# Kernel optimization log

Measured on AMD Instinct MI355X. Metric: run time of the kernel, lower is better.

Reference implementation:

```python
import jax, jax.numpy as jnp
import numpy as np
from jax import lax

K = 3
K2 = K * K
PAD = 1          # dcn padding = kernel_size // 2
OFF_DIL = 2      # offset conv dilation & padding
GN_GROUPS = 32
EPS = 1e-5


def setup_inputs() -> dict:
    key = jax.random.key(0)
    ks = jax.random.split(key, 4)
    B, C1, C2, H, W = 4, 256, 256, 64, 64
    x = jax.random.normal(ks[0], (B, C1, H, W), jnp.float32)
    # offset conv params (zero-init in module; small random here so deformable
    # sampling is genuinely irregular)
    w_off = jax.random.normal(ks[1], (3 * K2, C1, K, K), jnp.float32) * 0.01
    b_off = jax.random.normal(ks[2], (3 * K2,), jnp.float32) * 0.01
    # dcn weight, bias=False
    w_dcn = jax.random.normal(ks[3], (C2, C1, K, K), jnp.float32) * (1.0 / np.sqrt(C1 * K2))
    gamma = jnp.ones((C2,), jnp.float32)
    beta = jnp.zeros((C2,), jnp.float32)
    return {"x": x, "w_off": w_off, "b_off": b_off, "w_dcn": w_dcn,
            "gamma": gamma, "beta": beta}


def _dcnv2_block(x, w_off, b_off, w_dcn, gamma, beta):
    B, C, H, W = x.shape
    C2 = w_dcn.shape[0]

    # ---- offset/mask prediction: 3x3 conv, dilation=2, padding=2, stride=1 ----
    out_off = lax.conv_general_dilated(
        x, w_off, window_strides=(1, 1), padding=[(OFF_DIL, OFF_DIL)] * 2,
        rhs_dilation=(OFF_DIL, OFF_DIL),
        dimension_numbers=("NCHW", "OIHW", "NCHW"))
    out_off = out_off + b_off[None, :, None, None]

    offset = jnp.nan_to_num(jnp.clip(out_off[:, :2 * K2], -64.0, 64.0))
    mask = jax.nn.sigmoid(out_off[:, 2 * K2:])                     # [B,K2,H,W]

    off = offset.reshape(B, K2, 2, H, W)                            # (dy,dx) pairs per kernel pt
    dy, dx = off[:, :, 0], off[:, :, 1]                             # [B,K2,H,W]

    # ---- sampling positions: p0 + pk + offset (stride=1, pad=1, dil=1) ----
    ii = (jnp.arange(K2) // K).astype(jnp.float32)                  # kernel row
    jj = (jnp.arange(K2) % K).astype(jnp.float32)                   # kernel col
    yo = jnp.arange(H, dtype=jnp.float32)
    xo = jnp.arange(W, dtype=jnp.float32)
    py = yo[None, None, :, None] - PAD + ii[None, :, None, None] + dy   # [B,K2,H,W]
    px = xo[None, None, None, :] - PAD + jj[None, :, None, None] + dx

    y0 = jnp.floor(py)
    x0 = jnp.floor(px)
    wy = py - y0                                                    # frac weights
    wx = px - x0
    y0i = y0.astype(jnp.int32)
    x0i = x0.astype(jnp.int32)

    xf = x.reshape(B, C, H * W)

    def gather(yi, xi):
        # zero outside image (torchvision zero-padding bilinear semantics)
        valid = (yi >= 0) & (yi < H) & (xi >= 0) & (xi < W)
        idx = jnp.clip(yi, 0, H - 1) * W + jnp.clip(xi, 0, W - 1)   # [B,K2,H,W]
        v = jax.vmap(lambda xb, ib: xb[:, ib])(xf, idx.reshape(B, -1))  # [B,C,K2*H*W]
        v = v.reshape(B, C, K2, H, W)
        return v * valid[:, None].astype(x.dtype)

    v00 = gather(y0i, x0i)
    v01 = gather(y0i, x0i + 1)
    v10 = gather(y0i + 1, x0i)
    v11 = gather(y0i + 1, x0i + 1)

    wy_ = wy[:, None]
    wx_ = wx[:, None]
    samp = (v00 * (1 - wy_) * (1 - wx_) + v01 * (1 - wy_) * wx_
            + v10 * wy_ * (1 - wx_) + v11 * wy_ * wx_)              # [B,C,K2,H,W]
    samp = samp * mask[:, None]                                     # modulated (DCNv2)

    out = jnp.einsum("bckhw,dck->bdhw", samp, w_dcn.reshape(C2, C, K2))

    # ---- GroupNorm(32, C2) + SiLU ----
    G = GN_GROUPS
    o = out.reshape(B, G, C2 // G, H, W)
    mu = o.mean(axis=(2, 3, 4), keepdims=True)
    var = o.var(axis=(2, 3, 4), keepdims=True)
    o = (o - mu) * lax.rsqrt(var + EPS)
    out = o.reshape(B, C2, H, W) * gamma[None, :, None, None] + beta[None, :, None, None]
    return out * jax.nn.sigmoid(out)


def reference(x, w_off, b_off, w_dcn, gamma, beta):
    return _dcnv2_block(x, w_off, b_off, w_dcn, gamma, beta)
```

## Files before the change

kernel.cpp:

```cpp
#include <hip/hip_runtime.h>
#include <math.h>

#define HW 4096

typedef __attribute__((ext_vector_type(8))) short short8;
typedef __attribute__((ext_vector_type(4))) float f32x4;

static __device__ inline ushort f2bf(float f) {
    uint u = __builtin_bit_cast(uint, f);
    uint r = (u + 0x7fffu + ((u >> 16) & 1u)) >> 16;
    return (ushort)r;
}

__global__ __launch_bounds__(256) void k0_xt(const float* __restrict__ x, ushort* __restrict__ xt)
{
    const int blk = blockIdx.x;
    const int b = blk >> 6, h = blk & 63;
    __shared__ ushort tile[64 * 258];
    const float* xb = x + ((size_t)b * 256) * HW + h * 64;
    const int t = threadIdx.x;
    for (int e = t; e < 16384; e += 256) {
        const int c = e >> 6, j = e & 63;
        tile[j * 258 + c] = f2bf(xb[c * HW + j]);
    }
    __syncthreads();
    uint* xo = (uint*)(xt + ((size_t)b * HW + h * 64) * 256);
    for (int e = t; e < 8192; e += 256) {
        const int j = e >> 7, q = e & 127;
        xo[j * 128 + q] = *(const uint*)&tile[j * 258 + 2 * q];
    }
}

__global__ __launch_bounds__(256) void k0_wt(const float* __restrict__ w_dcn, ushort* __restrict__ wT)
{
    const int e = blockIdx.x * 256 + threadIdx.x;
    const int k = e >> 16, d = (e >> 8) & 255, c = e & 255;
    wT[e] = f2bf(w_dcn[(d * 256 + c) * 9 + k]);
}

__global__ __launch_bounds__(256) void k0_wo(const float* __restrict__ w_off, ushort* __restrict__ wA)
{
    const int e = blockIdx.x * 256 + threadIdx.x;
    const int k = e >> 13, r = e & 8191;
    const int oc = r >> 8, c = r & 255;
    const float v = (oc < 27) ? w_off[(oc * 256 + c) * 9 + k] : 0.f;
    wA[e] = f2bf(v);
}

__global__ __launch_bounds__(256) void k1_mfma(const ushort* __restrict__ xt,
    const ushort* __restrict__ wA, const float* __restrict__ b_off,
    float* __restrict__ offs, float* __restrict__ mk)
{
    const int bid = blockIdx.x;
    const int b = bid >> 6, h = bid & 63;
    const int t = threadIdx.x;
    const int lane = t & 63, wv = t >> 6;
    const int n = lane & 15, kq = lane >> 4;

    f32x4 acc0 = {0.f, 0.f, 0.f, 0.f}, acc1 = {0.f, 0.f, 0.f, 0.f};
    const ushort* xb = xt + ((size_t)b * HW) * 256;

    for (int k = 0; k < 9; ++k) {
        const int i = k / 3, j = k % 3;
        const int hh = h + 2 * (i - 1);
        if ((unsigned)hh >= 64u) continue;
        const int ww = wv * 16 + n + 2 * (j - 1);
        const bool vw = (unsigned)ww < 64u;
        const ushort* xrow  = xb + (hh * 64 + ww) * 256 + kq * 8;
        const ushort* wrow0 = wA + (k * 32 + n) * 256 + kq * 8;
        const ushort* wrow1 = wrow0 + 16 * 256;
#pragma unroll
        for (int c0 = 0; c0 < 256; c0 += 32) {
            short8 bfv = {0, 0, 0, 0, 0, 0, 0, 0};
            if (vw) bfv = *(const short8*)(xrow + c0);
            const short8 a0 = *(const short8*)(wrow0 + c0);
            const short8 a1 = *(const short8*)(wrow1 + c0);
            acc0 = __builtin_amdgcn_mfma_f32_16x16x32_bf16(a0, bfv, acc0, 0, 0, 0);
            acc1 = __builtin_amdgcn_mfma_f32_16x16x32_bf16(a1, bfv, acc1, 0, 0, 0);
        }
    }

    const int hw = h * 64 + wv * 16 + n;
#pragma unroll
    for (int r = 0; r < 4; ++r) {
        {
            const int oc = kq * 4 + r;
            float v = acc0[r] + b_off[oc];
            v = fminf(fmaxf(v, -64.f), 64.f);
            offs[(b * 18 + oc) * HW + hw] = v;
        }
        {
            const int oc = 16 + kq * 4 + r;
            const float v = acc1[r] + b_off[min(oc, 26)];
            if (oc < 18) {
                offs[(b * 18 + oc) * HW + hw] = fminf(fmaxf(v, -64.f), 64.f);
            } else if (oc < 27) {
                mk[(b * 9 + (oc - 18)) * HW + hw] = 1.f / (1.f + expf(-v));
            }
        }
    }
}

__global__ __launch_bounds__(1024) void k2_dcn(const ushort* __restrict__ xt, const ushort* __restrict__ wT,
    const float* __restrict__ offs, const float* __restrict__ mk, float* __restrict__ out)
{
    const int bid = blockIdx.x;
    const int wg = (bid & 7) * 32 + (bid >> 3);
    const int b = wg >> 6, h = wg & 63;
    const int t = threadIdx.x;

    __shared__ int4   cOff[576];
    __shared__ float4 cWgt[576];
    __shared__ ushort Alds[256 * 40];
    __shared__ ushort Slds[64 * 40];

    if (t < 576) {
        const int k = t >> 6, ww = t & 63;
        const float dy = offs[(b * 18 + 2 * k) * HW + h * 64 + ww];
        const float dx = offs[(b * 18 + 2 * k + 1) * HW + h * 64 + ww];
        const float mval = mk[(b * 9 + k) * HW + h * 64 + ww];
        const float py = (float)(h - 1 + k / 3) + dy;
        const float px = (float)(ww - 1 + k % 3) + dx;
        const float y0f = floorf(py), x0f = floorf(px);
        const float wy = py - y0f, wx = px - x0f;
        const int y0 = (int)y0f, x0 = (int)x0f;
        float w00 = (1.f - wy) * (1.f - wx) * mval, w01 = (1.f - wy) * wx * mval;
        float w10 = wy * (1.f - wx) * mval,         w11 = wy * wx * mval;
        const bool vy0 = (unsigned)y0 < 64u, vy1 = (unsigned)(y0 + 1) < 64u;
        const bool vx0 = (unsigned)x0 < 64u, vx1 = (unsigned)(x0 + 1) < 64u;
        if (!(vy0 && vx0)) w00 = 0.f;
        if (!(vy0 && vx1)) w01 = 0.f;
        if (!(vy1 && vx0)) w10 = 0.f;
        if (!(vy1 && vx1)) w11 = 0.f;
        const int y0c = min(max(y0, 0), 63), y1c = min(max(y0 + 1, 0), 63);
        const int x0c = min(max(x0, 0), 63), x1c = min(max(x0 + 1, 0), 63);
        cOff[t] = make_int4((y0c * 64 + x0c) * 512, (y0c * 64 + x1c) * 512,
                            (y1c * 64 + x0c) * 512, (y1c * 64 + x1c) * 512);
        cWgt[t] = make_float4(w00, w01, w10, w11);
    }

    f32x4 acc[4];
#pragma unroll
    for (int nf = 0; nf < 4; ++nf) acc[nf] = (f32x4){0.f, 0.f, 0.f, 0.f};

    const char* xc = (const char*)(xt + ((size_t)b * HW) * 256);
    const int lane = t & 63;
    const int d0 = (t >> 6) * 16;
    const int n0 = lane & 15, kb = (lane >> 4) * 8;
    const int sd = t >> 2, sq = t & 3;
    const int sw = t >> 4, sp = t & 15;

    __syncthreads();

    for (int k = 0; k < 9; ++k) {
        const int4   co = cOff[k * 64 + sw];
        const float4 cw = cWgt[k * 64 + sw];
        for (int c0 = 0; c0 < 256; c0 += 32) {
            __syncthreads();
            {
                const short8 av = *(const short8*)(wT + ((k * 256 + sd) * 256 + c0 + sq * 8));
                *(short8*)(&Alds[sd * 40 + sq * 8]) = av;
            }
            {
                const int cb = (c0 + sp * 2) * 2;
                const uint u00 = *(const uint*)(xc + (co.x + cb));
                const uint u01 = *(const uint*)(xc + (co.y + cb));
                const uint u10 = *(const uint*)(xc + (co.z + cb));
                const uint u11 = *(const uint*)(xc + (co.w + cb));
                const float sa = cw.x * __builtin_bit_cast(float, u00 << 16)
                               + cw.y * __builtin_bit_cast(float, u01 << 16)
                               + cw.z * __builtin_bit_cast(float, u10 << 16)
                               + cw.w * __builtin_bit_cast(float, u11 << 16);
                const float sb = cw.x * __builtin_bit_cast(float, u00 & 0xffff0000u)
                               + cw.y * __builtin_bit_cast(float, u01 & 0xffff0000u)
                               + cw.z * __builtin_bit_cast(float, u10 & 0xffff0000u)
                               + cw.w * __builtin_bit_cast(float, u11 & 0xffff0000u);
                ((uint*)Slds)[sw * 20 + sp] = (uint)f2bf(sa) | ((uint)f2bf(sb) << 16);
            }
            __syncthreads();
            const short8 af = *(const short8*)(&Alds[(d0 + n0) * 40 + kb]);
#pragma unroll
            for (int nf = 0; nf < 4; ++nf) {
                const short8 bf = *(const short8*)(&Slds[(nf * 16 + n0) * 40 + kb]);
                acc[nf] = __builtin_amdgcn_mfma_f32_16x16x32_bf16(af, bf, acc[nf], 0, 0, 0);
            }
        }
    }

    float* ob = out + ((size_t)b * 256) * HW + h * 64;
#pragma unroll
    for (int nf = 0; nf < 4; ++nf)
#pragma unroll
        for (int r = 0; r < 4; ++r) {
            const int d = d0 + (lane >> 4) * 4 + r;
            ob[d * HW + nf * 16 + n0] = acc[nf][r];
        }
}

__global__ __launch_bounds__(256) void k3_stats(const float* __restrict__ out, float* __restrict__ stats)
{
    const int bg = blockIdx.x;
    const float* p = out + (size_t)bg * 32768;
    float s = 0.f, s2 = 0.f;
    for (int i = threadIdx.x; i < 8192; i += 256) {
        float4 v = ((const float4*)p)[i];
        s  += v.x + v.y + v.z + v.w;
        s2 += v.x * v.x + v.y * v.y + v.z * v.z + v.w * v.w;
    }
    __shared__ float r1[256], r2[256];
    r1[threadIdx.x] = s; r2[threadIdx.x] = s2;
    __syncthreads();
    for (int st = 128; st > 0; st >>= 1) {
        if (threadIdx.x < st) {
            r1[threadIdx.x] += r1[threadIdx.x + st];
            r2[threadIdx.x] += r2[threadIdx.x + st];
        }
        __syncthreads();
    }
    if (threadIdx.x == 0) {
        const float mean = r1[0] / 32768.f;
        const float var  = r2[0] / 32768.f - mean * mean;
        stats[bg * 2]     = mean;
        stats[bg * 2 + 1] = rsqrtf(var + 1e-5f);
    }
}

__global__ __launch_bounds__(256) void k4_gn(float* __restrict__ out,
    const float* __restrict__ stats, const float* __restrict__ gamma, const float* __restrict__ beta)
{
    const int i4 = blockIdx.x * 256 + threadIdx.x;
    const int elem = i4 << 2;
    const int b = elem >> 20;
    const int ch = (elem >> 12) & 255;
    const int g = ch >> 3;
    const float mean = stats[(b * 32 + g) * 2];
    const float rstd = stats[(b * 32 + g) * 2 + 1];
    const float ga = gamma[ch], be = beta[ch];
    float4 v = ((float4*)out)[i4];
    float vv[4] = {v.x, v.y, v.z, v.w};
#pragma unroll
    for (int j = 0; j < 4; ++j) {
        const float o = (vv[j] - mean) * rstd * ga + be;
        vv[j] = o / (1.f + expf(-o));
    }
    ((float4*)out)[i4] = make_float4(vv[0], vv[1], vv[2], vv[3]);
}

extern "C" void kernel_launch(void* const* d_in, const int* in_sizes, int n_in,
                              void* d_out, int out_size, void* d_ws, size_t ws_size,
                              hipStream_t stream)
{
    const float* x     = (const float*)d_in[0];
    const float* w_off = (const float*)d_in[1];
    const float* b_off = (const float*)d_in[2];
    const float* w_dcn = (const float*)d_in[3];
    const float* gamma = (const float*)d_in[4];
    const float* beta  = (const float*)d_in[5];
    float* out = (float*)d_out;

    ushort* xt    = (ushort*)d_ws;
    float*  offs  = (float*)d_ws + 2097152;
    float*  mk    = offs + 294912;
    float*  stats = mk + 147456;
    ushort* wT    = (ushort*)(stats + 256);
    ushort* wA    = wT + 589824;

    hipLaunchKernelGGL(k0_xt,    dim3(256),  dim3(256),  0, stream, x, xt);
    hipLaunchKernelGGL(k0_wt,    dim3(2304), dim3(256),  0, stream, w_dcn, wT);
    hipLaunchKernelGGL(k0_wo,    dim3(288),  dim3(256),  0, stream, w_off, wA);
    hipLaunchKernelGGL(k1_mfma,  dim3(256),  dim3(256),  0, stream, xt, wA, b_off, offs, mk);
    hipLaunchKernelGGL(k2_dcn,   dim3(256),  dim3(1024), 0, stream, xt, wT, offs, mk, out);
    hipLaunchKernelGGL(k3_stats, dim3(128),  dim3(256),  0, stream, out, stats);
    hipLaunchKernelGGL(k4_gn,    dim3(4096), dim3(256),  0, stream, out, stats, gamma, beta);
}
```

Baseline: 209.9 us.

## Restructure DCN kernel with double-buffered sampled tiles, split-K offset conv, coalesced weight transpose

The main DCN kernel now samples a full 64x256 bf16 tile per kernel point into a double-buffered, XOR-swizzled LDS buffer. It builds the next point's tile while running MFMAs on the current one, so it needs one barrier per kernel point instead of two per 32-channel chunk. A-operand weights are read straight from global memory, and each wave computes a 32x64 output tile with 512 threads. The offset conv splits the channel reduction across two wave halves and reduces through LDS, and the weight transpose stages each output row in shared memory so reads are coalesced. In exchange, LDS use and register pressure per block go up, and the A-operand reads from global memory may not be reused well.

```diff
diff --git a/kernel.cpp b/kernel.cpp
--- a/kernel.cpp
+++ b/kernel.cpp
@@ -8,8 +8,10 @@
 
 static __device__ inline ushort f2bf(float f) {
     uint u = __builtin_bit_cast(uint, f);
-    uint r = (u + 0x7fffu + ((u >> 16) & 1u)) >> 16;
-    return (ushort)r;
+    return (ushort)((u + 0x7fffu + ((u >> 16) & 1u)) >> 16);
+}
+static __device__ inline float bf2f(ushort s) {
+    return __builtin_bit_cast(float, (uint)s << 16);
 }
 
 __global__ __launch_bounds__(256) void k0_xt(const float* __restrict__ x, ushort* __restrict__ xt)
@@ -33,9 +35,15 @@
 
 __global__ __launch_bounds__(256) void k0_wt(const float* __restrict__ w_dcn, ushort* __restrict__ wT)
 {
-    const int e = blockIdx.x * 256 + threadIdx.x;
-    const int k = e >> 16, d = (e >> 8) & 255, c = e & 255;
-    wT[e] = f2bf(w_dcn[(d * 256 + c) * 9 + k]);
+    const int d = blockIdx.x;
+    __shared__ float wl[2304];
+    const int t = threadIdx.x;
+    for (int i = t; i < 2304; i += 256) wl[i] = w_dcn[d * 2304 + i];
+    __syncthreads();
+    for (int i = t; i < 2304; i += 256) {
+        const int k = i >> 8, c = i & 255;
+        wT[k * 65536 + d * 256 + c] = f2bf(wl[c * 9 + k]);
+    }
 }
 
 __global__ __launch_bounds__(256) void k0_wo(const float* __restrict__ w_off, ushort* __restrict__ wA)
@@ -47,7 +55,7 @@
     wA[e] = f2bf(v);
 }
 
-__global__ __launch_bounds__(256) void k1_mfma(const ushort* __restrict__ xt,
+__global__ __launch_bounds__(512) void k1_mfma(const ushort* __restrict__ xt,
     const ushort* __restrict__ wA, const float* __restrict__ b_off,
     float* __restrict__ offs, float* __restrict__ mk)
 {
@@ -55,22 +63,25 @@
     const int b = bid >> 6, h = bid & 63;
     const int t = threadIdx.x;
     const int lane = t & 63, wv = t >> 6;
+    const int wq = wv & 3, chalf = wv >> 2;
     const int n = lane & 15, kq = lane >> 4;
+    __shared__ float red[4][64][8];
 
     f32x4 acc0 = {0.f, 0.f, 0.f, 0.f}, acc1 = {0.f, 0.f, 0.f, 0.f};
     const ushort* xb = xt + ((size_t)b * HW) * 256;
+    const int cb = chalf * 128;
 
     for (int k = 0; k < 9; ++k) {
         const int i = k / 3, j = k % 3;
         const int hh = h + 2 * (i - 1);
         if ((unsigned)hh >= 64u) continue;
-        const int ww = wv * 16 + n + 2 * (j - 1);
+        const int ww = wq * 16 + n + 2 * (j - 1);
         const bool vw = (unsigned)ww < 64u;
-        const ushort* xrow  = xb + (hh * 64 + ww) * 256 + kq * 8;
-        const ushort* wrow0 = wA + (k * 32 + n) * 256 + kq * 8;
+        const ushort* xrow  = xb + (hh * 64 + ww) * 256 + cb + kq * 8;
+        const ushort* wrow0 = wA + (k * 32 + n) * 256 + cb + kq * 8;
         const ushort* wrow1 = wrow0 + 16 * 256;
 #pragma unroll
-        for (int c0 = 0; c0 < 256; c0 += 32) {
+        for (int c0 = 0; c0 < 128; c0 += 32) {
             short8 bfv = {0, 0, 0, 0, 0, 0, 0, 0};
             if (vw) bfv = *(const short8*)(xrow + c0);
             const short8 a0 = *(const short8*)(wrow0 + c0);
@@ -80,47 +91,74 @@
         }
     }
 
-    const int hw = h * 64 + wv * 16 + n;
-#pragma unroll
-    for (int r = 0; r < 4; ++r) {
-        {
-            const int oc = kq * 4 + r;
-            float v = acc0[r] + b_off[oc];
-            v = fminf(fmaxf(v, -64.f), 64.f);
-            offs[(b * 18 + oc) * HW + hw] = v;
-        }
-        {
-            const int oc = 16 + kq * 4 + r;
-            const float v = acc1[r] + b_off[min(oc, 26)];
-            if (oc < 18) {
-                offs[(b * 18 + oc) * HW + hw] = fminf(fmaxf(v, -64.f), 64.f);
-            } else if (oc < 27) {
-                mk[(b * 9 + (oc - 18)) * HW + hw] = 1.f / (1.f + expf(-v));
-            }
-        }
-    }
-}
-
-__global__ __launch_bounds__(1024) void k2_dcn(const ushort* __restrict__ xt, const ushort* __restrict__ wT,
+    if (chalf == 1) {
+#pragma unroll
+        for (int r = 0; r < 4; ++r) {
+            red[wq][lane][r]     = acc0[r];
+            red[wq][lane][4 + r] = acc1[r];
+        }
+    }
+    __syncthreads();
+    if (chalf == 0) {
+#pragma unroll
+        for (int r = 0; r < 4; ++r) {
+            acc0[r] += red[wq][lane][r];
+            acc1[r] += red[wq][lane][4 + r];
+        }
+        const int hw = h * 64 + wq * 16 + n;
+#pragma unroll
+        for (int r = 0; r < 4; ++r) {
+            {
+                const int oc = kq * 4 + r;
+                float v = acc0[r] + b_off[oc];
+                v = fminf(fmaxf(v, -64.f), 64.f);
+                offs[(b * 18 + oc) * HW + hw] = v;
+            }
+            {
+                const int oc = 16 + kq * 4 + r;
+                const float v = acc1[r] + b_off[min(oc, 26)];
+                if (oc < 18) {
+                    offs[(b * 18 + oc) * HW + hw] = fminf(fmaxf(v, -64.f), 64.f);
+                } else if (oc < 27) {
+                    mk[(b * 9 + (oc - 18)) * HW + hw] = 1.f / (1.f + expf(-v));
+                }
+            }
+        }
+    }
+}
+
+__global__ __launch_bounds__(512) void k2_dcn(const ushort* __restrict__ xt, const ushort* __restrict__ wT,
     const float* __restrict__ offs, const float* __restrict__ mk, float* __restrict__ out)
 {
     const int bid = blockIdx.x;
     const int wg = (bid & 7) * 32 + (bid >> 3);
     const int b = wg >> 6, h = wg & 63;
     const int t = threadIdx.x;
-
-    __shared__ int4   cOff[576];
-    __shared__ float4 cWgt[576];
-    __shared__ ushort Alds[256 * 40];
-    __shared__ ushort Slds[64 * 40];
-
-    if (t < 576) {
-        const int k = t >> 6, ww = t & 63;
-        const float dy = offs[(b * 18 + 2 * k) * HW + h * 64 + ww];
-        const float dx = offs[(b * 18 + 2 * k + 1) * HW + h * 64 + ww];
-        const float mval = mk[(b * 9 + k) * HW + h * 64 + ww];
+    const int lane = t & 63, wv = t >> 6;
+    const int n0 = lane & 15, kq = lane >> 4;
+
+    __shared__ __align__(16) ushort S[2][16384];
+
+    const int sw = t >> 3;
+    const int so = (t & 7) * 4;
+    const int cbyte = (t & 7) * 64;
+
+    const char* xc = (const char*)(xt + ((size_t)b * HW) * 256);
+    const float* offb = offs + (size_t)b * 18 * HW + h * 64;
+    const float* mkb  = mk   + (size_t)b *  9 * HW + h * 64;
+
+    f32x4 acc[2][4];
+#pragma unroll
+    for (int dr = 0; dr < 2; ++dr)
+#pragma unroll
+        for (int nf = 0; nf < 4; ++nf) acc[dr][nf] = (f32x4){0.f, 0.f, 0.f, 0.f};
+
+    auto stage = [&](int k, int pb) {
+        const float dy = offb[(2 * k) * HW + sw];
+        const float dx = offb[(2 * k + 1) * HW + sw];
+        const float mval = mkb[k * HW + sw];
         const float py = (float)(h - 1 + k / 3) + dy;
-        const float px = (float)(ww - 1 + k % 3) + dx;
+        const float px = (float)(sw - 1 + k % 3) + dx;
         const float y0f = floorf(py), x0f = floorf(px);
         const float wy = py - y0f, wx = px - x0f;
         const int y0 = (int)y0f, x0 = (int)x0f;
@@ -134,67 +172,64 @@
         if (!(vy1 && vx1)) w11 = 0.f;
         const int y0c = min(max(y0, 0), 63), y1c = min(max(y0 + 1, 0), 63);
         const int x0c = min(max(x0, 0), 63), x1c = min(max(x0 + 1, 0), 63);
-        cOff[t] = make_int4((y0c * 64 + x0c) * 512, (y0c * 64 + x1c) * 512,
-                            (y1c * 64 + x0c) * 512, (y1c * 64 + x1c) * 512);
-        cWgt[t] = make_float4(w00, w01, w10, w11);
-    }
-
-    f32x4 acc[4];
-#pragma unroll
-    for (int nf = 0; nf < 4; ++nf) acc[nf] = (f32x4){0.f, 0.f, 0.f, 0.f};
-
-    const char* xc = (const char*)(xt + ((size_t)b * HW) * 256);
-    const int lane = t & 63;
-    const int d0 = (t >> 6) * 16;
-    const int n0 = lane & 15, kb = (lane >> 4) * 8;
-    const int sd = t >> 2, sq = t & 3;
-    const int sw = t >> 4, sp = t & 15;
-
-    __syncthreads();
-
+        const int o00 = (y0c * 64 + x0c) * 512, o01 = (y0c * 64 + x1c) * 512;
+        const int o10 = (y1c * 64 + x0c) * 512, o11 = (y1c * 64 + x1c) * 512;
+#pragma unroll
+        for (int j = 0; j < 4; ++j) {
+            const int cb2 = cbyte + j * 16;
+            const short8 u00 = *(const short8*)(xc + o00 + cb2);
+            const short8 u01 = *(const short8*)(xc + o01 + cb2);
+            const short8 u10 = *(const short8*)(xc + o10 + cb2);
+            const short8 u11 = *(const short8*)(xc + o11 + cb2);
+            short8 r;
+#pragma unroll
+            for (int e = 0; e < 8; ++e) {
+                const float v = w00 * bf2f((ushort)u00[e]) + w01 * bf2f((ushort)u01[e])
+                              + w10 * bf2f((ushort)u10[e]) + w11 * bf2f((ushort)u11[e]);
+                r[e] = (short)f2bf(v);
+            }
+            const int oct = so + j;
+            *(short8*)&S[pb][sw * 256 + ((oct ^ (sw & 7)) << 3)] = r;
+        }
+    };
+
+    auto gemm = [&](int k, int pb) {
+        const ushort* Arow0 = wT + k * 65536 + (wv * 32 + n0) * 256 + kq * 8;
+        const ushort* Arow1 = Arow0 + 16 * 256;
+#pragma unroll
+        for (int c0 = 0; c0 < 256; c0 += 32) {
+            const short8 a0 = *(const short8*)(Arow0 + c0);
+            const short8 a1 = *(const short8*)(Arow1 + c0);
+#pragma unroll
+            for (int nf = 0; nf < 4; ++nf) {
+                const int w = nf * 16 + n0;
+                const int oct = (c0 >> 3) + kq;
+                const short8 bf = *(const short8*)&S[pb][w * 256 + ((oct ^ (w & 7)) << 3)];
+                acc[0][nf] = __builtin_amdgcn_mfma_f32_16x16x32_bf16(a0, bf, acc[0][nf], 0, 0, 0);
+                acc[1][nf] = __builtin_amdgcn_mfma_f32_16x16x32_bf16(a1, bf, acc[1][nf], 0, 0, 0);
+            }
+        }
+    };
+
+    stage(0, 0);
+    __syncthreads();
+#pragma unroll 1
     for (int k = 0; k < 9; ++k) {
-        const int4   co = cOff[k * 64 + sw];
-        const float4 cw = cWgt[k * 64 + sw];
-        for (int c0 = 0; c0 < 256; c0 += 32) {
-            __syncthreads();
-            {
-                const short8 av = *(const short8*)(wT + ((k * 256 + sd) * 256 + c0 + sq * 8));
-                *(short8*)(&Alds[sd * 40 + sq * 8]) = av;
-            }
-            {
-                const int cb = (c0 + sp * 2) * 2;
-                const uint u00 = *(const uint*)(xc + (co.x + cb));
-                const uint u01 = *(const uint*)(xc + (co.y + cb));
-                const uint u10 = *(const uint*)(xc + (co.z + cb));
-                const uint u11 = *(const uint*)(xc + (co.w + cb));
-                const float sa = cw.x * __builtin_bit_cast(float, u00 << 16)
-                               + cw.y * __builtin_bit_cast(float, u01 << 16)
-                               + cw.z * __builtin_bit_cast(float, u10 << 16)
-                               + cw.w * __builtin_bit_cast(float, u11 << 16);
-                const float sb = cw.x * __builtin_bit_cast(float, u00 & 0xffff0000u)
-                               + cw.y * __builtin_bit_cast(float, u01 & 0xffff0000u)
-                               + cw.z * __builtin_bit_cast(float, u10 & 0xffff0000u)
-                               + cw.w * __builtin_bit_cast(float, u11 & 0xffff0000u);
-                ((uint*)Slds)[sw * 20 + sp] = (uint)f2bf(sa) | ((uint)f2bf(sb) << 16);
-            }
-            __syncthreads();
-            const short8 af = *(const short8*)(&Alds[(d0 + n0) * 40 + kb]);
-#pragma unroll
-            for (int nf = 0; nf < 4; ++nf) {
-                const short8 bf = *(const short8*)(&Slds[(nf * 16 + n0) * 40 + kb]);
-                acc[nf] = __builtin_amdgcn_mfma_f32_16x16x32_bf16(af, bf, acc[nf], 0, 0, 0);
-            }
-        }
+        if (k < 8) stage(k + 1, (k + 1) & 1);
+        gemm(k, k & 1);
+        __syncthreads();
     }
 
     float* ob = out + ((size_t)b * 256) * HW + h * 64;
 #pragma unroll
-    for (int nf = 0; nf < 4; ++nf)
-#pragma unroll
-        for (int r = 0; r < 4; ++r) {
-            const int d = d0 + (lane >> 4) * 4 + r;
-            ob[d * HW + nf * 16 + n0] = acc[nf][r];
-        }
+    for (int dr = 0; dr < 2; ++dr)
+#pragma unroll
+        for (int nf = 0; nf < 4; ++nf)
+#pragma unroll
+            for (int r = 0; r < 4; ++r) {
+                const int d = wv * 32 + dr * 16 + kq * 4 + r;
+                ob[(size_t)d * HW + nf * 16 + n0] = acc[dr][nf][r];
+            }
 }
 
 __global__ __launch_bounds__(256) void k3_stats(const float* __restrict__ out, float* __restrict__ stats)
@@ -265,11 +300,11 @@
     ushort* wT    = (ushort*)(stats + 256);
     ushort* wA    = wT + 589824;
 
-    hipLaunchKernelGGL(k0_xt,    dim3(256),  dim3(256),  0, stream, x, xt);
-    hipLaunchKernelGGL(k0_wt,    dim3(2304), dim3(256),  0, stream, w_dcn, wT);
-    hipLaunchKernelGGL(k0_wo,    dim3(288),  dim3(256),  0, stream, w_off, wA);
-    hipLaunchKernelGGL(k1_mfma,  dim3(256),  dim3(256),  0, stream, xt, wA, b_off, offs, mk);
-    hipLaunchKernelGGL(k2_dcn,   dim3(256),  dim3(1024), 0, stream, xt, wT, offs, mk, out);
-    hipLaunchKernelGGL(k3_stats, dim3(128),  dim3(256),  0, stream, out, stats);
-    hipLaunchKernelGGL(k4_gn,    dim3(4096), dim3(256),  0, stream, out, stats, gamma, beta);
-}
+    hipLaunchKernelGGL(k0_xt,    dim3(256),  dim3(256), 0, stream, x, xt);
+    hipLaunchKernelGGL(k0_wt,    dim3(256),  dim3(256), 0, stream, w_dcn, wT);
+    hipLaunchKernelGGL(k0_wo,    dim3(288),  dim3(256), 0, stream, w_off, wA);
+    hipLaunchKernelGGL(k1_mfma,  dim3(256),  dim3(512), 0, stream, xt, wA, b_off, offs, mk);
+    hipLaunchKernelGGL(k2_dcn,   dim3(256),  dim3(512), 0, stream, xt, wT, offs, mk, out);
+    hipLaunchKernelGGL(k3_stats, dim3(128),  dim3(256), 0, stream, out, stats);
+    hipLaunchKernelGGL(k4_gn,    dim3(4096), dim3(256), 0, stream, out, stats, gamma, beta);
+}
```

Result: faster. 195.9 us (-6.7%).
